# Kernel tuning notes

Hardware: AMD Instinct MI355X
Metric: run time of the kernel (lower is better)

Reference implementation:

```python
import jax, jax.numpy as jnp
import numpy as np

BATCH = 512
MODES = 256
WIDTH = 256  # modes == width required by the `x @ weights[1]` contraction


def crelu(z):
    # torch.relu is undefined on complex; the evident intent is componentwise relu
    return jax.nn.relu(z.real) + 1j * jax.nn.relu(z.imag)


def setup_inputs() -> dict:
    key = jax.random.key(0)
    ks = jax.random.split(key, 7)
    x = jax.random.normal(ks[0], (BATCH, MODES), dtype=jnp.float32)
    w0 = jax.random.normal(ks[1], (MODES, WIDTH), dtype=jnp.float32)
    w1 = jax.random.normal(ks[2], (MODES, WIDTH), dtype=jnp.float32)
    s = 1.0 / np.sqrt(WIDTH)
    lin1_w = jax.random.uniform(ks[3], (WIDTH, WIDTH), jnp.float32, -s, s)
    lin1_b = jax.random.uniform(ks[4], (WIDTH,), jnp.float32, -s, s)
    lin2_w = jax.random.uniform(ks[5], (WIDTH, WIDTH), jnp.float32, -s, s)
    lin2_b = jax.random.uniform(ks[6], (WIDTH,), jnp.float32, -s, s)
    return {"x": x, "w0": w0, "w1": w1,
            "lin1_w": lin1_w, "lin1_b": lin1_b,
            "lin2_w": lin2_w, "lin2_b": lin2_b}


def reference(x, w0, w1, lin1_w, lin1_b, lin2_w, lin2_b):
    modes = w0.shape[0]
    # torch.fft.fftn defaults to all dims
    X = jnp.fft.fftn(x)                                   # (B, modes) complex64
    # mode-wise lift: x.unsqueeze(-1) (*) weights[0]
    h = X[..., None] * w0                                 # (B, modes, width)
    h = crelu(h)
    # L = diag(exp(i 2pi n / modes)); dense L @ h == diagonal elementwise multiply
    phase = jnp.exp(1j * (2.0 * np.pi / modes)
                    * jnp.arange(modes, dtype=jnp.float32))  # (modes,) complex64
    h = phase[:, None] * h                                # (B, modes, width)
    # x @ weights[1]: contracts h's width dim with weights[1]'s first dim (modes==width)
    h = jnp.einsum('bmw,wv->bmv', h, w1.astype(h.dtype))  # (B, modes, width)
    h = h @ lin1_w.T.astype(h.dtype) + lin1_b             # Linear(width, width)
    h = crelu(h)
    h = h @ lin2_w.T.astype(h.dtype) + lin2_b             # Linear(width, width)
    return jnp.fft.ifftn(h)                               # (B, modes, width) complex64
```

## Files before the change

kernel.cpp:

```cpp
#include <hip/hip_runtime.h>
#include <hip/hip_bf16.h>


typedef unsigned short ushort_t;
typedef unsigned int   uint_t;
typedef __attribute__((ext_vector_type(8))) short short8b;
typedef __attribute__((ext_vector_type(4))) float f32x4;

__device__ __forceinline__ uint_t packf2(float lo, float hi){
  union { __hip_bfloat162 h; uint_t u; } v;
  v.h = __float22bfloat162_rn(make_float2(lo, hi));
  return v.u;
}
__device__ __forceinline__ ushort_t f2bf(float f){
  union { __hip_bfloat16 h; ushort_t u; } v;
  v.h = __float2bfloat16(f);
  return v.u;
}
__device__ __forceinline__ float bf_lo(uint_t u){
  union { uint_t u; float f; } v; v.u = u << 16; return v.f;
}
__device__ __forceinline__ float bf_hi(uint_t u){
  union { uint_t u; float f; } v; v.u = u & 0xFFFF0000u; return v.f;
}
__device__ __forceinline__ void gld16(const void* g, void* l){
  __builtin_amdgcn_global_load_lds(
      (const __attribute__((address_space(1))) void*)g,
      (__attribute__((address_space(3))) void*)l, 16, 0, 0);
}

constexpr int BR16T[16] = {0,8,4,12,2,10,6,14,1,9,5,13,3,11,7,15};
constexpr int BR32T[32] = {0,16,8,24,4,20,12,28,2,18,10,26,6,22,14,30,
                           1,17,9,25,5,21,13,29,3,19,11,27,7,23,15,31};

__device__ __forceinline__ void bfly(float& ar, float& ai, float& br, float& bi,
                                     float wr, float wi){
  float sr = ar - br, si = ai - bi;
  ar += br; ai += bi;
  br = sr*wr - si*wi;
  bi = sr*wi + si*wr;
}

__device__ __forceinline__ void fft16_inv(float* xr, float* xi){
  const float C1 = 0.92387953251128674f, S1 = 0.38268343236508978f,
              C2 = 0.70710678118654752f;
  bfly(xr[0],xi[0],xr[8],xi[8],    1.f, 0.f);
  bfly(xr[1],xi[1],xr[9],xi[9],    C1,  S1);
  bfly(xr[2],xi[2],xr[10],xi[10],  C2,  C2);
  bfly(xr[3],xi[3],xr[11],xi[11],  S1,  C1);
  bfly(xr[4],xi[4],xr[12],xi[12],  0.f, 1.f);
  bfly(xr[5],xi[5],xr[13],xi[13], -S1,  C1);
  bfly(xr[6],xi[6],xr[14],xi[14], -C2,  C2);
  bfly(xr[7],xi[7],xr[15],xi[15], -C1,  S1);
  #pragma unroll
  for (int h = 0; h < 16; h += 8){
    bfly(xr[h+0],xi[h+0],xr[h+4],xi[h+4],  1.f, 0.f);
    bfly(xr[h+1],xi[h+1],xr[h+5],xi[h+5],  C2,  C2);
    bfly(xr[h+2],xi[h+2],xr[h+6],xi[h+6],  0.f, 1.f);
    bfly(xr[h+3],xi[h+3],xr[h+7],xi[h+7], -C2,  C2);
  }
  #pragma unroll
  for (int h = 0; h < 16; h += 4){
    bfly(xr[h+0],xi[h+0],xr[h+2],xi[h+2], 1.f, 0.f);
    bfly(xr[h+1],xi[h+1],xr[h+3],xi[h+3], 0.f, 1.f);
  }
  #pragma unroll
  for (int h = 0; h < 16; h += 2)
    bfly(xr[h],xi[h],xr[h+1],xi[h+1], 1.f, 0.f);
}

__device__ __forceinline__ void fft32_inv(float* xr, float* xi){
  constexpr float WR[16] = {
    1.f, 0.98078528040323044f, 0.92387953251128674f, 0.83146961230254524f,
    0.70710678118654752f, 0.55557023301960222f, 0.38268343236508978f, 0.19509032201612827f,
    0.f,-0.19509032201612827f,-0.38268343236508978f,-0.55557023301960222f,
   -0.70710678118654752f,-0.83146961230254524f,-0.92387953251128674f,-0.98078528040323044f};
  constexpr float WI[16] = {
    0.f, 0.19509032201612827f, 0.38268343236508978f, 0.55557023301960222f,
    0.70710678118654752f, 0.83146961230254524f, 0.92387953251128674f, 0.98078528040323044f,
    1.f, 0.98078528040323044f, 0.92387953251128674f, 0.83146961230254524f,
    0.70710678118654752f, 0.55557023301960222f, 0.38268343236508978f, 0.19509032201612827f};
  #pragma unroll
  for (int j = 0; j < 16; ++j)
    bfly(xr[j],xi[j],xr[j+16],xi[j+16], WR[j], WI[j]);
  fft16_inv(xr, xi);
  fft16_inv(xr+16, xi+16);
}

__global__ void fill_tables(float2* t256f, float2* t256i, float2* t512f, float2* t512i){
  int i = threadIdx.x;
  const double PI2 = 6.283185307179586476925286766559;
  if (i < 256){
    double a = PI2 * (double)i / 256.0;
    float c = (float)cos(a), s = (float)sin(a);
    t256f[i] = make_float2(c, -s);
    t256i[i] = make_float2(c,  s);
  }
  {
    double a = PI2 * (double)i / 512.0;
    float c = (float)cos(a), s = (float)sin(a);
    t512f[i] = make_float2(c, -s);
    t512i[i] = make_float2(c,  s);
  }
}

__global__ void dft_m(const float* __restrict__ x, float2* __restrict__ Yw,
                      const float2* __restrict__ twf){
  __shared__ float xs[256];
  __shared__ float2 tws[256];
  int b = blockIdx.x, k = threadIdx.x;
  xs[k]  = x[b*256 + k];
  tws[k] = twf[k];
  __syncthreads();
  float yr = 0.f, yi = 0.f;
  for (int m = 0; m < 256; ++m){
    float2 w = tws[(m*k) & 255];
    float xv = xs[m];
    yr += xv*w.x; yi += xv*w.y;
  }
  Yw[b*256 + k] = make_float2(yr, yi);
}

__global__ void dft_b(const float2* __restrict__ Yw, float* __restrict__ Xr,
                      float* __restrict__ Xi, const float2* __restrict__ twf){
  __shared__ float2 tws[512];
  int j = blockIdx.x, k = threadIdx.x;
  tws[k]       = twf[k];
  tws[k + 256] = twf[k + 256];
  __syncthreads();
  float xr = 0.f, xi = 0.f;
  for (int b = 0; b < 512; ++b){
    float2 y = Yw[b*256 + k];
    float2 w = tws[(b*j) & 511];
    xr += y.x*w.x - y.y*w.y;
    xi += y.x*w.y + y.y*w.x;
  }
  Xr[j*256 + k] = xr;
  Xi[j*256 + k] = xi;
}

__global__ void prep_w(const float* __restrict__ w1, const float* __restrict__ lin1_w,
                       ushort_t* __restrict__ Wct){
  __shared__ float l1[256];
  int u = blockIdx.x, t = threadIdx.x;
  l1[t] = lin1_w[u*256 + t];
  __syncthreads();
  float s = 0.f;
  for (int v = 0; v < 256; ++v)
    s += l1[v] * w1[t*256 + v];
  Wct[u*256 + t] = f2bf(s);
}

__global__ void prep_g(const float* __restrict__ lin2_w, const float2* __restrict__ ph,
                       ushort_t* __restrict__ BtR, ushort_t* __restrict__ BtI){
  int v = blockIdx.x, k = threadIdx.x;
  float cre = 0.f, cim = 0.f;
  for (int u = 0; u < 256; ++u){
    float w = lin2_w[u*256 + k];
    float2 t = ph[(u*v) & 255];
    cre += w*t.x; cim += w*t.y;
  }
  BtR[v*256 + k] = f2bf(cre * (1.f/256.f));
  BtI[v*256 + k] = f2bf(cim * (1.f/256.f));
}

__global__ void prep_b2g(const float* __restrict__ b2, const float2* __restrict__ ph,
                         float2* __restrict__ b2g){
  int v = threadIdx.x;
  float cre = 0.f, cim = 0.f;
  for (int u = 0; u < 256; ++u){
    float w = b2[u];
    float2 t = ph[(u*v) & 255];
    cre += w*t.x; cim += w*t.y;
  }
  b2g[v] = make_float2(cre * (1.f/256.f), cim * (1.f/256.f));
}

__global__ __launch_bounds__(512, 4)
void fused_mid(const float* __restrict__ Xr, const float* __restrict__ Xi,
               const float* __restrict__ w0,
               const ushort_t* __restrict__ Wct,
               const ushort_t* __restrict__ BtR, const ushort_t* __restrict__ BtI,
               const float* __restrict__ b1, const float2* __restrict__ b2g,
               const float2* __restrict__ ph,
               uint_t* __restrict__ OutP)
{
  __shared__ __align__(16) char lds[65536];
  ushort_t* H3 = (ushort_t*)(lds + 32768);

  const int tid  = threadIdx.x;
  const int lane = tid & 63;
  const int w8   = tid >> 6;
  const int L    = lane & 15;
  const int chk  = lane >> 4;
  const int cq   = chk, cl = L;
  const int cr0  = blockIdx.x * 32;

  const int arow = tid >> 3;
  const int ak0  = (tid & 7) * 4;
  const int ajj  = arow & 31;
  const bool aim = arow >= 32;
  const float axr = Xr[cr0 + ajj];
  const float axi = Xi[cr0 + ajj];
  const float2 apj = ph[(cr0 + ajj) & 255];
  const int am = (cr0 + ajj) & 255;
  const int aslot = (ak0 >> 3) ^ ((arow >> 1) & 3);
  const int aoff  = arow*64 + aslot*16 + (ak0 & 7)*2;

  const int fsl  = chk ^ ((L >> 1) & 3);
  const int avix = L*32 + fsl*8;
  const int bvix = w8*1024 + avix;

  const int bc = (tid & 3) ^ ((tid >> 3) & 3);

  #define STAGE_B(W, kt, bsel) do {                                        \
    char* _d = lds + (bsel)*16384 + tid*16;                                \
    _Pragma("unroll")                                                      \
    for (int _i = 0; _i < 2; ++_i){                                        \
      int _row = _i*128 + (tid >> 2);                                      \
      gld16((W) + _row*256 + (kt)*32 + bc*8, _d + _i*8192);                \
    }                                                                      \
  } while(0)

  #define STAGE_A(kt, bsel) do {                                           \
    const float4 _w4 = *(const float4*)&w0[(size_t)am*256 + (kt)*32 + ak0];\
    float _wv[4] = {_w4.x, _w4.y, _w4.z, _w4.w};                           \
    float _va[4];                                                          \
    _Pragma("unroll")                                                      \
    for (int _e = 0; _e < 4; ++_e){                                        \
      float _r = fmaxf(axr*_wv[_e], 0.f);                                  \
      float _m = fmaxf(axi*_wv[_e], 0.f);                                  \
      _va[_e] = aim ? (apj.y*_r + apj.x*_m) : (apj.x*_r - apj.y*_m);       \
    }                                                                      \
    *(uint2*)(lds + 32768 + (bsel)*4096 + aoff) =                          \
        make_uint2(packf2(_va[0], _va[1]), packf2(_va[2], _va[3]));        \
  } while(0)

  f32x4 acc[4][2];
  #pragma unroll
  for (int m = 0; m < 4; ++m)
    #pragma unroll
    for (int n = 0; n < 2; ++n)
      acc[m][n] = (f32x4){0.f,0.f,0.f,0.f};

  int buf = 0;
  STAGE_B(Wct, 0, 0);
  STAGE_A(0, 0);
  __syncthreads();
  for (int kt = 0; kt < 8; ++kt){
    if (kt < 7){ STAGE_B(Wct, kt+1, buf^1); STAGE_A(kt+1, buf^1); }
    const ushort_t* Ab = (const ushort_t*)(lds + 32768 + buf*4096);
    const ushort_t* Bb = (const ushort_t*)(lds + buf*16384);
    short8b av[4], bv[2];
    #pragma unroll
    for (int m = 0; m < 4; ++m) av[m] = *(const short8b*)&Ab[avix + m*512];
    #pragma unroll
    for (int n = 0; n < 2; ++n) bv[n] = *(const short8b*)&Bb[bvix + n*512];
    #pragma unroll
    for (int m = 0; m < 4; ++m)
      #pragma unroll
      for (int n = 0; n < 2; ++n)
        acc[m][n] = __builtin_amdgcn_mfma_f32_16x16x32_bf16(av[m], bv[n], acc[m][n], 0,0,0);
    __syncthreads();
    buf ^= 1;
  }

  STAGE_B(BtR, 0, 0);
  #pragma unroll
  for (int m = 0; m < 4; ++m){
    #pragma unroll
    for (int n = 0; n < 2; ++n){
      int col = w8*32 + n*16 + cl;
      float badd = (m < 2) ? b1[col] : 0.f;
      #pragma unroll
      for (int q = 0; q < 4; ++q){
        int row = m*16 + cq*4 + q;
        float v = fmaxf(acc[m][n][q] + badd, 0.f);
        int s = (col >> 3) ^ (row & 7);
        H3[row*256 + s*8 + (col & 7)] = f2bf(v);
      }
    }
  }
  __syncthreads();

  f32x4 accR[4][2], accI[4][2];
  #pragma unroll
  for (int m = 0; m < 4; ++m)
    #pragma unroll
    for (int n = 0; n < 2; ++n){
      accR[m][n] = (f32x4){0.f,0.f,0.f,0.f};
      accI[m][n] = (f32x4){0.f,0.f,0.f,0.f};
    }

  buf = 0;
  for (int kp = 0; kp < 8; ++kp){
    short8b av[4], bv[2];
    #pragma unroll
    for (int m = 0; m < 4; ++m){
      int r = m*16 + L;
      int sl = (kp*4 + chk) ^ (r & 7);
      av[m] = *(const short8b*)&H3[r*256 + sl*8];
    }
    STAGE_B(BtI, kp, buf^1);
    {
      const ushort_t* Bb = (const ushort_t*)(lds + buf*16384);
      #pragma unroll
      for (int n = 0; n < 2; ++n) bv[n] = *(const short8b*)&Bb[bvix + n*512];
      #pragma unroll
      for (int m = 0; m < 4; ++m)
        #pragma unroll
        for (int n = 0; n < 2; ++n)
          accR[m][n] = __builtin_amdgcn_mfma_f32_16x16x32_bf16(av[m], bv[n], accR[m][n], 0,0,0);
    }
    __syncthreads();
    buf ^= 1;
    if (kp < 7) STAGE_B(BtR, kp+1, buf^1);
    {
      const ushort_t* Bb = (const ushort_t*)(lds + buf*16384);
      #pragma unroll
      for (int n = 0; n < 2; ++n) bv[n] = *(const short8b*)&Bb[bvix + n*512];
      #pragma unroll
      for (int m = 0; m < 4; ++m)
        #pragma unroll
        for (int n = 0; n < 2; ++n)
          accI[m][n] = __builtin_amdgcn_mfma_f32_16x16x32_bf16(av[m], bv[n], accI[m][n], 0,0,0);
    }
    __syncthreads();
    buf ^= 1;
  }

  #pragma unroll
  for (int n = 0; n < 2; ++n){
    int col = w8*32 + n*16 + cl;
    float2 bg = b2g[col];
    #pragma unroll
    for (int m2 = 0; m2 < 2; ++m2){
      #pragma unroll
      for (int q = 0; q < 4; ++q){
        int j = m2*16 + cq*4 + q;
        float vr = accR[m2][n][q]   - accI[m2+2][n][q] + bg.x;
        float vi = accI[m2][n][q]   + accR[m2+2][n][q] + bg.y;
        OutP[(long)(cr0 + j)*256 + col] = packf2(vr, vi);
      }
    }
  }
  #undef STAGE_B
  #undef STAGE_A
}

__global__ __launch_bounds__(512)
void fft_m(uint_t* __restrict__ P, const float2* __restrict__ ph){
  __shared__ uint_t Z[8192];
  const int tid = threadIdx.x;
  const int v  = tid & 31;
  const int bm = tid >> 5;
  const int bB = blockIdx.x >> 3;
  const int vg = (blockIdx.x & 7) << 5;
  const long base = (long)bB*65536 + vg + v;

  float xr[16], xi[16];
  #pragma unroll
  for (int a = 0; a < 16; ++a){
    uint_t u = P[base + (long)(a*16 + bm)*256];
    xr[a] = bf_lo(u); xi[a] = bf_hi(u);
  }
  fft16_inv(xr, xi);
  float2 ws = ph[bm];
  float wr = 1.f/256.f, wi = 0.f;
  #pragma unroll
  for (int d = 0; d < 16; ++d){
    float yr = xr[BR16T[d]], yi = xi[BR16T[d]];
    Z[d*512 + bm*32 + v] = packf2(yr*wr - yi*wi, yr*wi + yi*wr);
    float nw = wr*ws.x - wi*ws.y; wi = wr*ws.y + wi*ws.x; wr = nw;
  }
  __syncthreads();
  const int d2 = tid >> 5;
  float br[16], bi[16];
  #pragma unroll
  for (int bb = 0; bb < 16; ++bb){
    uint_t u = Z[d2*512 + bb*32 + v];
    br[bb] = bf_lo(u); bi[bb] = bf_hi(u);
  }
  fft16_inv(br, bi);
  #pragma unroll
  for (int p = 0; p < 16; ++p)
    P[base + (long)(BR16T[p]*16 + d2)*256] = packf2(br[p], bi[p]);
}

__global__ __launch_bounds__(512)
void fft_b(uint_t* __restrict__ P, const float2* __restrict__ t512){
  __shared__ uint_t Z[16384];
  const int tid = threadIdx.x;
  const int v  = tid & 31;
  const int bq = tid >> 5;
  const int m  = blockIdx.x >> 3;
  const int vg = (blockIdx.x & 7) << 5;
  const long base = (long)m*256 + vg + v;

  float xr[32], xi[32];
  #pragma unroll
  for (int a = 0; a < 32; ++a){
    uint_t u = P[base + (long)(a*16 + bq)*65536];
    xr[a] = bf_lo(u); xi[a] = bf_hi(u);
  }
  fft32_inv(xr, xi);
  float2 ws = t512[bq];
  float wr = 1.f/512.f, wi = 0.f;
  #pragma unroll
  for (int d = 0; d < 32; ++d){
    float yr = xr[BR32T[d]], yi = xi[BR32T[d]];
    Z[d*512 + bq*32 + v] = packf2(yr*wr - yi*wi, yr*wi + yi*wr);
    float nw = wr*ws.x - wi*ws.y; wi = wr*ws.y + wi*ws.x; wr = nw;
  }
  __syncthreads();
  float* out = (float*)P;
  #pragma unroll
  for (int h = 0; h < 2; ++h){
    const int d = (tid >> 5) + 16*h;
    float br[16], bi[16];
    #pragma unroll
    for (int bb = 0; bb < 16; ++bb){
      uint_t u = Z[d*512 + bb*32 + v];
      br[bb] = bf_lo(u); bi[bb] = bf_hi(u);
    }
    fft16_inv(br, bi);
    #pragma unroll
    for (int p = 0; p < 16; ++p)
      out[base + (long)(BR16T[p]*32 + d)*65536] = br[p];
  }
}

extern "C" void kernel_launch(void* const* d_in, const int* in_sizes, int n_in,
                              void* d_out, int out_size, void* d_ws, size_t ws_size,
                              hipStream_t stream) {
  (void)in_sizes; (void)n_in; (void)out_size; (void)ws_size;
  const float* x      = (const float*)d_in[0];
  const float* w0     = (const float*)d_in[1];
  const float* w1     = (const float*)d_in[2];
  const float* lin1_w = (const float*)d_in[3];
  const float* lin1_b = (const float*)d_in[4];
  const float* lin2_w = (const float*)d_in[5];
  const float* lin2_b = (const float*)d_in[6];

  char* sm = (char*)d_ws;
  float2*   Yw     = (float2*)sm;   sm += 1048576;
  float*    Xr     = (float*)sm;    sm += 524288;
  float*    Xi     = (float*)sm;    sm += 524288;
  float2*   t256f  = (float2*)sm;   sm += 2048;
  float2*   t256i  = (float2*)sm;   sm += 2048;
  float2*   t512f  = (float2*)sm;   sm += 4096;
  float2*   t512i  = (float2*)sm;   sm += 4096;
  ushort_t* Wct    = (ushort_t*)sm; sm += 131072;
  ushort_t* BtR    = (ushort_t*)sm; sm += 131072;
  ushort_t* BtI    = (ushort_t*)sm; sm += 131072;
  float2*   b2g    = (float2*)sm;   sm += 2048;

  uint_t* planes = (uint_t*)d_out;

  fill_tables<<<1, 512, 0, stream>>>(t256f, t256i, t512f, t512i);
  dft_m<<<512, 256, 0, stream>>>(x, Yw, t256f);
  dft_b<<<512, 256, 0, stream>>>(Yw, Xr, Xi, t512f);
  prep_w<<<256, 256, 0, stream>>>(w1, lin1_w, Wct);
  prep_g<<<256, 256, 0, stream>>>(lin2_w, t256i, BtR, BtI);
  prep_b2g<<<1, 256, 0, stream>>>(lin2_b, t256i, b2g);
  fused_mid<<<4096, 512, 0, stream>>>(Xr, Xi, w0, Wct, BtR, BtI, lin1_b, b2g,
                                      t256i, planes);
  fft_m<<<4096, 512, 0, stream>>>(planes, t256i);
  fft_b<<<2048, 512, 0, stream>>>(planes, t512i);
}
```

Before: 327.5 us.

## Load GEMM weights directly from global and widen FFT blocks

fused_mid no longer double-buffers the B weight tiles through LDS with global_load_lds and per-step barriers. It now precomputes the whole A tile into LDS once and has each wave read its weight fragments straight from global/L2. The second GEMM reads the real and imaginary weights together and issues both MFMAs per step. The FFT kernels move to 1024-thread blocks covering 64 columns, and fft_b processes its two halves in sequence through one shared buffer. This removes barriers and LDS staging but exposes global-load latency directly inside the MFMA loops.

```diff
diff --git a/kernel.cpp b/kernel.cpp
--- a/kernel.cpp
+++ b/kernel.cpp
@@ -22,11 +22,6 @@
 }
 __device__ __forceinline__ float bf_hi(uint_t u){
   union { uint_t u; float f; } v; v.u = u & 0xFFFF0000u; return v.f;
-}
-__device__ __forceinline__ void gld16(const void* g, void* l){
-  __builtin_amdgcn_global_load_lds(
-      (const __attribute__((address_space(1))) void*)g,
-      (__attribute__((address_space(3))) void*)l, 16, 0, 0);
 }
 
 constexpr int BR16T[16] = {0,8,4,12,2,10,6,14,1,9,5,13,3,11,7,15};
@@ -185,8 +180,8 @@
                const float2* __restrict__ ph,
                uint_t* __restrict__ OutP)
 {
-  __shared__ __align__(16) char lds[65536];
-  ushort_t* H3 = (ushort_t*)(lds + 32768);
+  __shared__ __align__(16) ushort_t At[64*256];
+  __shared__ __align__(16) ushort_t H3[64*256];
 
   const int tid  = threadIdx.x;
   const int lane = tid & 63;
@@ -196,45 +191,33 @@
   const int cq   = chk, cl = L;
   const int cr0  = blockIdx.x * 32;
 
-  const int arow = tid >> 3;
-  const int ak0  = (tid & 7) * 4;
-  const int ajj  = arow & 31;
-  const bool aim = arow >= 32;
-  const float axr = Xr[cr0 + ajj];
-  const float axi = Xi[cr0 + ajj];
-  const float2 apj = ph[(cr0 + ajj) & 255];
-  const int am = (cr0 + ajj) & 255;
-  const int aslot = (ak0 >> 3) ^ ((arow >> 1) & 3);
-  const int aoff  = arow*64 + aslot*16 + (ak0 & 7)*2;
-
-  const int fsl  = chk ^ ((L >> 1) & 3);
-  const int avix = L*32 + fsl*8;
-  const int bvix = w8*1024 + avix;
-
-  const int bc = (tid & 3) ^ ((tid >> 3) & 3);
-
-  #define STAGE_B(W, kt, bsel) do {                                        \
-    char* _d = lds + (bsel)*16384 + tid*16;                                \
-    _Pragma("unroll")                                                      \
-    for (int _i = 0; _i < 2; ++_i){                                        \
-      int _row = _i*128 + (tid >> 2);                                      \
-      gld16((W) + _row*256 + (kt)*32 + bc*8, _d + _i*8192);                \
-    }                                                                      \
-  } while(0)
-
-  #define STAGE_A(kt, bsel) do {                                           \
-    const float4 _w4 = *(const float4*)&w0[(size_t)am*256 + (kt)*32 + ak0];\
-    float _wv[4] = {_w4.x, _w4.y, _w4.z, _w4.w};                           \
-    float _va[4];                                                          \
-    _Pragma("unroll")                                                      \
-    for (int _e = 0; _e < 4; ++_e){                                        \
-      float _r = fmaxf(axr*_wv[_e], 0.f);                                  \
-      float _m = fmaxf(axi*_wv[_e], 0.f);                                  \
-      _va[_e] = aim ? (apj.y*_r + apj.x*_m) : (apj.x*_r - apj.y*_m);       \
-    }                                                                      \
-    *(uint2*)(lds + 32768 + (bsel)*4096 + aoff) =                          \
-        make_uint2(packf2(_va[0], _va[1]), packf2(_va[2], _va[3]));        \
-  } while(0)
+  {
+    const int arow = tid >> 3;
+    const int ak0  = (tid & 7) * 4;
+    const int ajj  = arow & 31;
+    const bool aim = arow >= 32;
+    const float axr = Xr[cr0 + ajj];
+    const float axi = Xi[cr0 + ajj];
+    const int am = (cr0 + ajj) & 255;
+    const float2 apj = ph[am];
+    #pragma unroll
+    for (int kt = 0; kt < 8; ++kt){
+      const int k = kt*32 + ak0;
+      const float4 w4 = *(const float4*)&w0[(size_t)am*256 + k];
+      float wv[4] = {w4.x, w4.y, w4.z, w4.w};
+      float va[4];
+      #pragma unroll
+      for (int e = 0; e < 4; ++e){
+        float r = fmaxf(axr*wv[e], 0.f);
+        float m = fmaxf(axi*wv[e], 0.f);
+        va[e] = aim ? (apj.y*r + apj.x*m) : (apj.x*r - apj.y*m);
+      }
+      int s = (k >> 3) ^ (arow & 7);
+      *(uint2*)((char*)At + arow*512 + s*16 + (ak0 & 7)*2) =
+          make_uint2(packf2(va[0], va[1]), packf2(va[2], va[3]));
+    }
+  }
+  __syncthreads();
 
   f32x4 acc[4][2];
   #pragma unroll
@@ -243,29 +226,26 @@
     for (int n = 0; n < 2; ++n)
       acc[m][n] = (f32x4){0.f,0.f,0.f,0.f};
 
-  int buf = 0;
-  STAGE_B(Wct, 0, 0);
-  STAGE_A(0, 0);
-  __syncthreads();
+  #pragma unroll
   for (int kt = 0; kt < 8; ++kt){
-    if (kt < 7){ STAGE_B(Wct, kt+1, buf^1); STAGE_A(kt+1, buf^1); }
-    const ushort_t* Ab = (const ushort_t*)(lds + 32768 + buf*4096);
-    const ushort_t* Bb = (const ushort_t*)(lds + buf*16384);
     short8b av[4], bv[2];
     #pragma unroll
-    for (int m = 0; m < 4; ++m) av[m] = *(const short8b*)&Ab[avix + m*512];
-    #pragma unroll
-    for (int n = 0; n < 2; ++n) bv[n] = *(const short8b*)&Bb[bvix + n*512];
+    for (int n = 0; n < 2; ++n){
+      int col = w8*32 + n*16 + L;
+      bv[n] = *(const short8b*)&Wct[col*256 + kt*32 + chk*8];
+    }
+    #pragma unroll
+    for (int m = 0; m < 4; ++m){
+      int row = m*16 + L;
+      av[m] = *(const short8b*)&At[row*256 + (((kt*4 + chk) ^ (L & 7)) << 3)];
+    }
     #pragma unroll
     for (int m = 0; m < 4; ++m)
       #pragma unroll
       for (int n = 0; n < 2; ++n)
         acc[m][n] = __builtin_amdgcn_mfma_f32_16x16x32_bf16(av[m], bv[n], acc[m][n], 0,0,0);
-    __syncthreads();
-    buf ^= 1;
-  }
-
-  STAGE_B(BtR, 0, 0);
+  }
+
   #pragma unroll
   for (int m = 0; m < 4; ++m){
     #pragma unroll
@@ -292,41 +272,28 @@
       accI[m][n] = (f32x4){0.f,0.f,0.f,0.f};
     }
 
-  buf = 0;
+  #pragma unroll
   for (int kp = 0; kp < 8; ++kp){
-    short8b av[4], bv[2];
+    short8b av[4], bR[2], bI[2];
+    #pragma unroll
+    for (int n = 0; n < 2; ++n){
+      int col = w8*32 + n*16 + L;
+      int off = col*256 + kp*32 + chk*8;
+      bR[n] = *(const short8b*)&BtR[off];
+      bI[n] = *(const short8b*)&BtI[off];
+    }
     #pragma unroll
     for (int m = 0; m < 4; ++m){
-      int r = m*16 + L;
-      int sl = (kp*4 + chk) ^ (r & 7);
-      av[m] = *(const short8b*)&H3[r*256 + sl*8];
-    }
-    STAGE_B(BtI, kp, buf^1);
-    {
-      const ushort_t* Bb = (const ushort_t*)(lds + buf*16384);
+      int row = m*16 + L;
+      av[m] = *(const short8b*)&H3[row*256 + (((kp*4 + chk) ^ (L & 7)) << 3)];
+    }
+    #pragma unroll
+    for (int m = 0; m < 4; ++m)
       #pragma unroll
-      for (int n = 0; n < 2; ++n) bv[n] = *(const short8b*)&Bb[bvix + n*512];
-      #pragma unroll
-      for (int m = 0; m < 4; ++m)
-        #pragma unroll
-        for (int n = 0; n < 2; ++n)
-          accR[m][n] = __builtin_amdgcn_mfma_f32_16x16x32_bf16(av[m], bv[n], accR[m][n], 0,0,0);
-    }
-    __syncthreads();
-    buf ^= 1;
-    if (kp < 7) STAGE_B(BtR, kp+1, buf^1);
-    {
-      const ushort_t* Bb = (const ushort_t*)(lds + buf*16384);
-      #pragma unroll
-      for (int n = 0; n < 2; ++n) bv[n] = *(const short8b*)&Bb[bvix + n*512];
-      #pragma unroll
-      for (int m = 0; m < 4; ++m)
-        #pragma unroll
-        for (int n = 0; n < 2; ++n)
-          accI[m][n] = __builtin_amdgcn_mfma_f32_16x16x32_bf16(av[m], bv[n], accI[m][n], 0,0,0);
-    }
-    __syncthreads();
-    buf ^= 1;
+      for (int n = 0; n < 2; ++n){
+        accR[m][n] = __builtin_amdgcn_mfma_f32_16x16x32_bf16(av[m], bR[n], accR[m][n], 0,0,0);
+        accI[m][n] = __builtin_amdgcn_mfma_f32_16x16x32_bf16(av[m], bI[n], accI[m][n], 0,0,0);
+      }
   }
 
   #pragma unroll
@@ -338,24 +305,22 @@
       #pragma unroll
       for (int q = 0; q < 4; ++q){
         int j = m2*16 + cq*4 + q;
-        float vr = accR[m2][n][q]   - accI[m2+2][n][q] + bg.x;
-        float vi = accI[m2][n][q]   + accR[m2+2][n][q] + bg.y;
+        float vr = accR[m2][n][q] - accI[m2+2][n][q] + bg.x;
+        float vi = accI[m2][n][q] + accR[m2+2][n][q] + bg.y;
         OutP[(long)(cr0 + j)*256 + col] = packf2(vr, vi);
       }
     }
   }
-  #undef STAGE_B
-  #undef STAGE_A
-}
-
-__global__ __launch_bounds__(512)
+}
+
+__global__ __launch_bounds__(1024)
 void fft_m(uint_t* __restrict__ P, const float2* __restrict__ ph){
-  __shared__ uint_t Z[8192];
+  __shared__ uint_t Z[16384];
   const int tid = threadIdx.x;
-  const int v  = tid & 31;
-  const int bm = tid >> 5;
-  const int bB = blockIdx.x >> 3;
-  const int vg = (blockIdx.x & 7) << 5;
+  const int v  = tid & 63;
+  const int bm = tid >> 6;
+  const int bB = blockIdx.x >> 2;
+  const int vg = (blockIdx.x & 3) << 6;
   const long base = (long)bB*65536 + vg + v;
 
   float xr[16], xi[16];
@@ -370,15 +335,15 @@
   #pragma unroll
   for (int d = 0; d < 16; ++d){
     float yr = xr[BR16T[d]], yi = xi[BR16T[d]];
-    Z[d*512 + bm*32 + v] = packf2(yr*wr - yi*wi, yr*wi + yi*wr);
+    Z[d*1024 + bm*64 + v] = packf2(yr*wr - yi*wi, yr*wi + yi*wr);
     float nw = wr*ws.x - wi*ws.y; wi = wr*ws.y + wi*ws.x; wr = nw;
   }
   __syncthreads();
-  const int d2 = tid >> 5;
+  const int d2 = tid >> 6;
   float br[16], bi[16];
   #pragma unroll
   for (int bb = 0; bb < 16; ++bb){
-    uint_t u = Z[d2*512 + bb*32 + v];
+    uint_t u = Z[d2*1024 + bb*64 + v];
     br[bb] = bf_lo(u); bi[bb] = bf_hi(u);
   }
   fft16_inv(br, bi);
@@ -387,14 +352,14 @@
     P[base + (long)(BR16T[p]*16 + d2)*256] = packf2(br[p], bi[p]);
 }
 
-__global__ __launch_bounds__(512)
+__global__ __launch_bounds__(1024)
 void fft_b(uint_t* __restrict__ P, const float2* __restrict__ t512){
   __shared__ uint_t Z[16384];
   const int tid = threadIdx.x;
-  const int v  = tid & 31;
-  const int bq = tid >> 5;
-  const int m  = blockIdx.x >> 3;
-  const int vg = (blockIdx.x & 7) << 5;
+  const int v  = tid & 63;
+  const int bq = tid >> 6;
+  const int m  = blockIdx.x >> 2;
+  const int vg = (blockIdx.x & 3) << 6;
   const long base = (long)m*256 + vg + v;
 
   float xr[32], xi[32];
@@ -406,27 +371,47 @@
   fft32_inv(xr, xi);
   float2 ws = t512[bq];
   float wr = 1.f/512.f, wi = 0.f;
-  #pragma unroll
-  for (int d = 0; d < 32; ++d){
+  float* out = (float*)P;
+  const int d2 = tid >> 6;
+
+  #pragma unroll
+  for (int d = 0; d < 16; ++d){
     float yr = xr[BR32T[d]], yi = xi[BR32T[d]];
-    Z[d*512 + bq*32 + v] = packf2(yr*wr - yi*wi, yr*wi + yi*wr);
+    Z[d*1024 + bq*64 + v] = packf2(yr*wr - yi*wi, yr*wi + yi*wr);
     float nw = wr*ws.x - wi*ws.y; wi = wr*ws.y + wi*ws.x; wr = nw;
   }
   __syncthreads();
-  float* out = (float*)P;
-  #pragma unroll
-  for (int h = 0; h < 2; ++h){
-    const int d = (tid >> 5) + 16*h;
+  {
     float br[16], bi[16];
     #pragma unroll
     for (int bb = 0; bb < 16; ++bb){
-      uint_t u = Z[d*512 + bb*32 + v];
+      uint_t u = Z[d2*1024 + bb*64 + v];
       br[bb] = bf_lo(u); bi[bb] = bf_hi(u);
     }
     fft16_inv(br, bi);
     #pragma unroll
     for (int p = 0; p < 16; ++p)
-      out[base + (long)(BR16T[p]*32 + d)*65536] = br[p];
+      out[base + (long)(BR16T[p]*32 + d2)*65536] = br[p];
+  }
+  __syncthreads();
+  #pragma unroll
+  for (int d = 16; d < 32; ++d){
+    float yr = xr[BR32T[d]], yi = xi[BR32T[d]];
+    Z[(d-16)*1024 + bq*64 + v] = packf2(yr*wr - yi*wi, yr*wi + yi*wr);
+    float nw = wr*ws.x - wi*ws.y; wi = wr*ws.y + wi*ws.x; wr = nw;
+  }
+  __syncthreads();
+  {
+    float br[16], bi[16];
+    #pragma unroll
+    for (int bb = 0; bb < 16; ++bb){
+      uint_t u = Z[d2*1024 + bb*64 + v];
+      br[bb] = bf_lo(u); bi[bb] = bf_hi(u);
+    }
+    fft16_inv(br, bi);
+    #pragma unroll
+    for (int p = 0; p < 16; ++p)
+      out[base + (long)(BR16T[p]*32 + (d2 + 16))*65536] = br[p];
   }
 }
 
@@ -465,6 +450,6 @@
   prep_b2g<<<1, 256, 0, stream>>>(lin2_b, t256i, b2g);
   fused_mid<<<4096, 512, 0, stream>>>(Xr, Xi, w0, Wct, BtR, BtI, lin1_b, b2g,
                                       t256i, planes);
-  fft_m<<<4096, 512, 0, stream>>>(planes, t256i);
-  fft_b<<<2048, 512, 0, stream>>>(planes, t512i);
-}
+  fft_m<<<2048, 1024, 0, stream>>>(planes, t256i);
+  fft_b<<<1024, 1024, 0, stream>>>(planes, t512i);
+}
```

Result: slower. 420.7 us, median of 5 (+28.5%).
